# Optimization experiments

Hardware: AMD Instinct MI355X
Metric: run time of the kernel (lower is better)

The kernel has to match this reference:

```python
import jax, jax.numpy as jnp
import numpy as np

NODE_DIM = 256
EDGE_H = 128
B, N = 2, 512
EPS = 1e-5

def _layernorm(x, g, b):
    mu = jnp.mean(x, axis=-1, keepdims=True)
    var = jnp.mean((x - mu) ** 2, axis=-1, keepdims=True)
    return (x - mu) * jax.lax.rsqrt(var + EPS) * g + b

def setup_inputs() -> dict:
    key = jax.random.key(0)
    ks = jax.random.split(key, 12)
    s = lambda k, shape, fan: jax.random.normal(k, shape, jnp.float32) * (1.0 / np.sqrt(fan))
    return {
        "latent_values": jax.random.normal(ks[0], (B, N, NODE_DIM), jnp.float32),
        "sn_g": jnp.ones((NODE_DIM,), jnp.float32),
        "sn_b": jnp.zeros((NODE_DIM,), jnp.float32),
        "tn_g": jnp.ones((NODE_DIM,), jnp.float32),
        "tn_b": jnp.zeros((NODE_DIM,), jnp.float32),
        "sW": s(ks[1], (EDGE_H, NODE_DIM), NODE_DIM),
        "sb": jnp.zeros((EDGE_H,), jnp.float32),
        "tW": s(ks[2], (EDGE_H, NODE_DIM), NODE_DIM),
        "tb": jnp.zeros((EDGE_H,), jnp.float32),
        "W1": s(ks[3], (EDGE_H, 3 * EDGE_H), 3 * EDGE_H),
        "b1": jnp.zeros((EDGE_H,), jnp.float32),
        "W2": s(ks[4], (1, EDGE_H), EDGE_H),
        "b2": jnp.zeros((1,), jnp.float32),
    }

def reference(latent_values, sn_g, sn_b, tn_g, tn_b, sW, sb, tW, tb, W1, b1, W2, b2):
    # projected source/target features: [B, N, H]
    src = _layernorm(latent_values, sn_g, sn_b) @ sW.T + sb
    tgt = _layernorm(latent_values, tn_g, tn_b) @ tW.T + tb
    # first MLP linear on concat([src_i, tgt_j, src_i*tgt_j]) decomposed into
    # three H-blocks of W1 -- same math, no 3H concat materialized.
    Ws, Wt, Wp = W1[:, :EDGE_H], W1[:, EDGE_H:2 * EDGE_H], W1[:, 2 * EDGE_H:]
    h = (src @ Ws.T)[:, :, None, :] + (tgt @ Wt.T)[:, None, :, :]
    h = h + jnp.einsum("bih,bjh,kh->bijk", src, tgt, Wp) + b1  # [B, N, N, H]
    h = jax.nn.gelu(h, approximate=False)
    logits = jnp.einsum("bijk,k->bij", h, W2[0]) + b2[0]
    edges = logits / (1.0 + jnp.abs(logits))  # softsign
    # mask self-edges (allow_self_edges=False)
    diag = jnp.eye(N, dtype=bool)
    return jnp.where(diag[None, :, :], 0.0, edges)
```

## Files before the change

### kernel.cpp

```cpp
#include <hip/hip_runtime.h>
#include <math.h>

#define BN 512
#define ND 256
#define EH 128

typedef __attribute__((ext_vector_type(8))) short short8v;
typedef __attribute__((ext_vector_type(4))) float f32x4;

__device__ __forceinline__ unsigned short f2bf_rn(float x) {
  unsigned int u = __float_as_uint(x);
  unsigned int r = u + 0x7FFFu + ((u >> 16) & 1u);
  return (unsigned short)(r >> 16);
}
__device__ __forceinline__ float bf2f(unsigned short h) {
  return __uint_as_float(((unsigned int)h) << 16);
}

__global__ __launch_bounds__(256) void prep_kernel(
    const float* __restrict__ latent,
    const float* __restrict__ sng, const float* __restrict__ snb,
    const float* __restrict__ tng, const float* __restrict__ tnb,
    const float* __restrict__ sW,  const float* __restrict__ sb,
    const float* __restrict__ tW,  const float* __restrict__ tbv,
    const float* __restrict__ W1,  const float* __restrict__ b1,
    float* __restrict__ srcg, float* __restrict__ apreg,
    unsigned short* __restrict__ tgtb)
{
  __shared__ float lns[4][256];
  __shared__ float lnt[4][256];
  __shared__ float ssrc[4][128];
  const int tid = threadIdx.x;
  const int w = tid >> 6, lane = tid & 63;
  const int row0 = blockIdx.x << 2;

  {
    const int row = row0 + w;
    const float* x = latent + (size_t)row * ND;
    const int h = lane << 2;
    float4 xv = *(const float4*)(x + h);
    float s1 = xv.x + xv.y + xv.z + xv.w;
    float s2 = xv.x*xv.x + xv.y*xv.y + xv.z*xv.z + xv.w*xv.w;
    #pragma unroll
    for (int m = 1; m < 64; m <<= 1) {
      s1 += __shfl_xor(s1, m, 64);
      s2 += __shfl_xor(s2, m, 64);
    }
    const float mu  = s1 * (1.0f/256.0f);
    const float var = s2 * (1.0f/256.0f) - mu*mu;
    const float rstd = rsqrtf(var + 1e-5f);
    float4 ga = *(const float4*)(sng + h), ba = *(const float4*)(snb + h);
    float4 gb = *(const float4*)(tng + h), bb = *(const float4*)(tnb + h);
    const float n0 = (xv.x - mu)*rstd, n1 = (xv.y - mu)*rstd;
    const float n2 = (xv.z - mu)*rstd, n3 = (xv.w - mu)*rstd;
    lns[w][h+0] = n0*ga.x + ba.x; lns[w][h+1] = n1*ga.y + ba.y;
    lns[w][h+2] = n2*ga.z + ba.z; lns[w][h+3] = n3*ga.w + ba.w;
    lnt[w][h+0] = n0*gb.x + bb.x; lnt[w][h+1] = n1*gb.y + bb.y;
    lnt[w][h+2] = n2*gb.z + bb.z; lnt[w][h+3] = n3*gb.w + bb.w;
  }
  __syncthreads();

  const int side = tid >> 7, k = tid & 127;
  {
    const float* W = side ? tW : sW;
    const float bias = side ? tbv[k] : sb[k];
    const float (*L)[256] = side ? lnt : lns;
    float a0 = bias, a1 = bias, a2 = bias, a3 = bias;
    const float* wr = W + (size_t)k * ND;
    for (int h4 = 0; h4 < ND; h4 += 4) {
      float4 wv = *(const float4*)(wr + h4);
      float4 l0 = *(const float4*)&L[0][h4];
      float4 l1 = *(const float4*)&L[1][h4];
      float4 l2 = *(const float4*)&L[2][h4];
      float4 l3 = *(const float4*)&L[3][h4];
      a0 += wv.x*l0.x + wv.y*l0.y + wv.z*l0.z + wv.w*l0.w;
      a1 += wv.x*l1.x + wv.y*l1.y + wv.z*l1.z + wv.w*l1.w;
      a2 += wv.x*l2.x + wv.y*l2.y + wv.z*l2.z + wv.w*l2.w;
      a3 += wv.x*l3.x + wv.y*l3.y + wv.z*l3.z + wv.w*l3.w;
    }
    if (!side) {
      ssrc[0][k]=a0; ssrc[1][k]=a1; ssrc[2][k]=a2; ssrc[3][k]=a3;
      srcg[(size_t)(row0+0)*EH+k]=a0; srcg[(size_t)(row0+1)*EH+k]=a1;
      srcg[(size_t)(row0+2)*EH+k]=a2; srcg[(size_t)(row0+3)*EH+k]=a3;
    } else {
      tgtb[(size_t)(row0+0)*EH + k] = f2bf_rn(a0);
      tgtb[(size_t)(row0+1)*EH + k] = f2bf_rn(a1);
      tgtb[(size_t)(row0+2)*EH + k] = f2bf_rn(a2);
      tgtb[(size_t)(row0+3)*EH + k] = f2bf_rn(a3);
    }
  }
  __syncthreads();

  {
    const int kk = tid & 127, half = tid >> 7;
    const float bb = b1[kk];
    float a0 = bb, a1 = bb;
    const float* wr = W1 + (size_t)kk * 384;
    const int r0 = half * 2;
    for (int h4 = 0; h4 < EH; h4 += 4) {
      float4 wv = *(const float4*)(wr + h4);
      float4 l0 = *(const float4*)&ssrc[r0][h4];
      float4 l1 = *(const float4*)&ssrc[r0+1][h4];
      a0 += wv.x*l0.x + wv.y*l0.y + wv.z*l0.z + wv.w*l0.w;
      a1 += wv.x*l1.x + wv.y*l1.y + wv.z*l1.z + wv.w*l1.w;
    }
    apreg[(size_t)(row0+r0)*EH + kk]   = a0;
    apreg[(size_t)(row0+r0+1)*EH + kk] = a1;
  }
}

__global__ __launch_bounds__(256, 2) void edge_kernel(
    const float* __restrict__ srcg, const float* __restrict__ apreg,
    const unsigned short* __restrict__ tgtb,
    const float* __restrict__ W1, const float* __restrict__ W2,
    const float* __restrict__ b2, float* __restrict__ out)
{
  __shared__ __align__(16) unsigned short Ghi[128 * 128];
  __shared__ __align__(16) unsigned short Glo[128 * 128];
  __shared__ float s_src[128];

  const int tid = threadIdx.x;
  const int l = tid & 63, w = tid >> 6;
  const int blk = blockIdx.x;
  const int b = blk >> 9, i = blk & 511;

  if (tid < 128) s_src[tid] = srcg[(size_t)blk * EH + tid];
  __syncthreads();

  {
    const int k = tid >> 1, h0 = (tid & 1) * 64;
    const float* wpr = W1 + (size_t)k * 384 + 256 + h0;
    const float* wtr = W1 + (size_t)k * 384 + 128 + h0;
    const unsigned int swz = (unsigned int)((k & 15) << 4);
    char* ghB = (char*)Ghi + k * 256;
    char* glB = (char*)Glo + k * 256;
    #pragma unroll
    for (int c = 0; c < 64; c += 8) {
      float4 wpa = *(const float4*)(wpr + c);
      float4 wpb = *(const float4*)(wpr + c + 4);
      float4 wta = *(const float4*)(wtr + c);
      float4 wtb = *(const float4*)(wtr + c + 4);
      float4 sa  = *(const float4*)&s_src[h0 + c];
      float4 sb4 = *(const float4*)&s_src[h0 + c + 4];
      float g[8];
      g[0] = fmaf(sa.x,  wpa.x, wta.x); g[1] = fmaf(sa.y,  wpa.y, wta.y);
      g[2] = fmaf(sa.z,  wpa.z, wta.z); g[3] = fmaf(sa.w,  wpa.w, wta.w);
      g[4] = fmaf(sb4.x, wpb.x, wtb.x); g[5] = fmaf(sb4.y, wpb.y, wtb.y);
      g[6] = fmaf(sb4.z, wpb.z, wtb.z); g[7] = fmaf(sb4.w, wpb.w, wtb.w);
      short8v hv, lv;
      #pragma unroll
      for (int q = 0; q < 8; ++q) {
        unsigned short hh = f2bf_rn(g[q]);
        hv[q] = (short)hh;
        lv[q] = (short)f2bf_rn(g[q] - bf2f(hh));
      }
      const unsigned int off = ((unsigned int)((h0 + c) * 2)) ^ swz;
      *(short8v*)(ghB + off) = hv;
      *(short8v*)(glB + off) = lv;
    }
  }
  __syncthreads();

  const int l15 = l & 15;
  const int hi4 = l >> 4;
  float apv[8], w2h[8];
  #pragma unroll
  for (int nt = 0; nt < 8; ++nt) {
    apv[nt] = apreg[(size_t)blk * EH + nt * 16 + l15];
    w2h[nt] = 0.5f * W2[nt * 16 + l15];
  }
  const float b2s = b2[0];

  const unsigned short* tB = tgtb + (size_t)b * BN * EH;
  float* orow = out + (size_t)blk * BN;

  const int cb = hi4 * 16;
  const unsigned int swzl = (unsigned int)(l15 << 4);

#define LOADA(buf, ks_)                                                        \
  {                                                                            \
    _Pragma("unroll")                                                          \
    for (int m = 0; m < 4; ++m) {                                              \
      const size_t r = (size_t)(jt0 + m * 16 + l15) * EH + (ks_) * 32 + hi4 * 8;\
      buf[m] = *(const short8v*)(tB + r);                                      \
    }                                                                          \
  }

#define MFMA_STEP(buf, ks_)                                                    \
  {                                                                            \
    _Pragma("unroll")                                                          \
    for (int nt = 0; nt < 8; ++nt) {                                           \
      const int rowoff = nt * 4096 + l15 * 256;                                \
      const unsigned int col = ((unsigned int)(((ks_) << 6) | cb)) ^ swzl;     \
      short8v bhi = *(const short8v*)((const char*)Ghi + rowoff + col);        \
      short8v blo = *(const short8v*)((const char*)Glo + rowoff + col);        \
      _Pragma("unroll")                                                        \
      for (int m = 0; m < 4; ++m) {                                            \
        acc[m][nt] = __builtin_amdgcn_mfma_f32_16x16x32_bf16(buf[m], bhi, acc[m][nt], 0, 0, 0); \
        acc[m][nt] = __builtin_amdgcn_mfma_f32_16x16x32_bf16(buf[m], blo, acc[m][nt], 0, 0, 0); \
      }                                                                        \
    }                                                                          \
  }

  #pragma unroll 1
  for (int p = 0; p < 2; ++p) {
    const int jt0 = (w * 8 + p * 4) * 16;
    f32x4 acc[4][8];
    #pragma unroll
    for (int m = 0; m < 4; ++m)
      #pragma unroll
      for (int nt = 0; nt < 8; ++nt)
        acc[m][nt] = (f32x4){0.f, 0.f, 0.f, 0.f};

    short8v aA[4], aB[4];
    LOADA(aA, 0)
    #pragma unroll 1
    for (int kk = 0; kk < 2; ++kk) {
      const int ks0 = kk * 2;
      LOADA(aB, ks0 + 1)
      MFMA_STEP(aA, ks0)
      if (kk == 0) LOADA(aA, 2)
      MFMA_STEP(aB, ks0 + 1)
    }

    #pragma unroll
    for (int m = 0; m < 4; ++m) {
      #pragma unroll
      for (int reg = 0; reg < 4; ++reg) {
        float ps = 0.0f;
        #pragma unroll
        for (int nt = 0; nt < 8; ++nt) {
          const float x = acc[m][nt][reg] + apv[nt];
          const float e  = __builtin_amdgcn_exp2f(x * x * -0.7213475204f);
          const float t  = __builtin_amdgcn_rcpf(fmaf(0.33267817f, fabsf(x), 1.0f));
          const float pl = t * fmaf(t, fmaf(t, 0.7478556f, -0.0958798f), 0.3480242f);
          const float u  = x * (pl * e);
          const float tw = fmaf(2.0f, x, -u);
          const float g2 = (x < 0.0f) ? u : tw;
          ps = fmaf(w2h[nt], g2, ps);
        }
        ps += __shfl_xor(ps, 1, 64);
        ps += __shfl_xor(ps, 2, 64);
        ps += __shfl_xor(ps, 4, 64);
        ps += __shfl_xor(ps, 8, 64);
        if (l15 == 0) {
          const int j = jt0 + m * 16 + hi4 * 4 + reg;
          const float s = ps + b2s;
          const float e2 = s / (1.0f + fabsf(s));
          orow[j] = (j == i) ? 0.0f : e2;
        }
      }
    }
  }
#undef LOADA
#undef MFMA_STEP
}

extern "C" void kernel_launch(void* const* d_in, const int* in_sizes, int n_in,
                              void* d_out, int out_size, void* d_ws, size_t ws_size,
                              hipStream_t stream) {
  const float* latent = (const float*)d_in[0];
  const float* sng = (const float*)d_in[1];
  const float* snb = (const float*)d_in[2];
  const float* tng = (const float*)d_in[3];
  const float* tnb = (const float*)d_in[4];
  const float* sW  = (const float*)d_in[5];
  const float* sb  = (const float*)d_in[6];
  const float* tW  = (const float*)d_in[7];
  const float* tb  = (const float*)d_in[8];
  const float* W1  = (const float*)d_in[9];
  const float* b1  = (const float*)d_in[10];
  const float* W2  = (const float*)d_in[11];
  const float* b2  = (const float*)d_in[12];
  float* out = (float*)d_out;

  float* ws = (float*)d_ws;
  float* srcg  = ws;
  float* apreg = ws + 131072;
  unsigned short* tgtb = (unsigned short*)(ws + 262144);

  hipLaunchKernelGGL(prep_kernel, dim3(256), dim3(256), 0, stream,
                     latent, sng, snb, tng, tnb, sW, sb, tW, tb, W1, b1,
                     srcg, apreg, tgtb);
  hipLaunchKernelGGL(edge_kernel, dim3(1024), dim3(256), 0, stream,
                     srcg, apreg, tgtb, W1, W2, b2, out);
}
```

Before: 84.13 us.

## Drop bf16 hi/lo split, use tanh-approx GELU, shrink tiles for occupancy

Removes the low-order bf16 correction term for the W1-derived B operand, which halves the MFMA count and the LDS footprint. The exact-erf GELU polynomial is replaced by a sigmoid-based tanh approximation. Tiles shrink to 2 M-subtiles with 4 passes, allowing four waves per SIMD, and the apre bias is folded into the accumulator initialisation. Outputs are now written as float4. The cost is lower numerical accuracy from the single bf16 product and the approximate GELU, which may exceed tolerance.

```diff
diff --git a/kernel.cpp b/kernel.cpp
--- a/kernel.cpp
+++ b/kernel.cpp
@@ -109,14 +109,13 @@
   }
 }
 
-__global__ __launch_bounds__(256, 2) void edge_kernel(
+__global__ __launch_bounds__(256, 4) void edge_kernel(
     const float* __restrict__ srcg, const float* __restrict__ apreg,
     const unsigned short* __restrict__ tgtb,
     const float* __restrict__ W1, const float* __restrict__ W2,
     const float* __restrict__ b2, float* __restrict__ out)
 {
-  __shared__ __align__(16) unsigned short Ghi[128 * 128];
-  __shared__ __align__(16) unsigned short Glo[128 * 128];
+  __shared__ __align__(16) unsigned short Gs[128 * 128];
   __shared__ float s_src[128];
 
   const int tid = threadIdx.x;
@@ -132,8 +131,7 @@
     const float* wpr = W1 + (size_t)k * 384 + 256 + h0;
     const float* wtr = W1 + (size_t)k * 384 + 128 + h0;
     const unsigned int swz = (unsigned int)((k & 15) << 4);
-    char* ghB = (char*)Ghi + k * 256;
-    char* glB = (char*)Glo + k * 256;
+    char* gB = (char*)Gs + k * 256;
     #pragma unroll
     for (int c = 0; c < 64; c += 8) {
       float4 wpa = *(const float4*)(wpr + c);
@@ -142,32 +140,28 @@
       float4 wtb = *(const float4*)(wtr + c + 4);
       float4 sa  = *(const float4*)&s_src[h0 + c];
       float4 sb4 = *(const float4*)&s_src[h0 + c + 4];
-      float g[8];
-      g[0] = fmaf(sa.x,  wpa.x, wta.x); g[1] = fmaf(sa.y,  wpa.y, wta.y);
-      g[2] = fmaf(sa.z,  wpa.z, wta.z); g[3] = fmaf(sa.w,  wpa.w, wta.w);
-      g[4] = fmaf(sb4.x, wpb.x, wtb.x); g[5] = fmaf(sb4.y, wpb.y, wtb.y);
-      g[6] = fmaf(sb4.z, wpb.z, wtb.z); g[7] = fmaf(sb4.w, wpb.w, wtb.w);
-      short8v hv, lv;
-      #pragma unroll
-      for (int q = 0; q < 8; ++q) {
-        unsigned short hh = f2bf_rn(g[q]);
-        hv[q] = (short)hh;
-        lv[q] = (short)f2bf_rn(g[q] - bf2f(hh));
-      }
+      short8v hv;
+      hv[0] = (short)f2bf_rn(fmaf(sa.x,  wpa.x, wta.x));
+      hv[1] = (short)f2bf_rn(fmaf(sa.y,  wpa.y, wta.y));
+      hv[2] = (short)f2bf_rn(fmaf(sa.z,  wpa.z, wta.z));
+      hv[3] = (short)f2bf_rn(fmaf(sa.w,  wpa.w, wta.w));
+      hv[4] = (short)f2bf_rn(fmaf(sb4.x, wpb.x, wtb.x));
+      hv[5] = (short)f2bf_rn(fmaf(sb4.y, wpb.y, wtb.y));
+      hv[6] = (short)f2bf_rn(fmaf(sb4.z, wpb.z, wtb.z));
+      hv[7] = (short)f2bf_rn(fmaf(sb4.w, wpb.w, wtb.w));
       const unsigned int off = ((unsigned int)((h0 + c) * 2)) ^ swz;
-      *(short8v*)(ghB + off) = hv;
-      *(short8v*)(glB + off) = lv;
+      *(short8v*)(gB + off) = hv;
     }
   }
   __syncthreads();
 
   const int l15 = l & 15;
   const int hi4 = l >> 4;
-  float apv[8], w2h[8];
+  float apv[8], w2v[8];
   #pragma unroll
   for (int nt = 0; nt < 8; ++nt) {
     apv[nt] = apreg[(size_t)blk * EH + nt * 16 + l15];
-    w2h[nt] = 0.5f * W2[nt * 16 + l15];
+    w2v[nt] = W2[nt * 16 + l15];
   }
   const float b2s = b2[0];
 
@@ -180,7 +174,7 @@
 #define LOADA(buf, ks_)                                                        \
   {                                                                            \
     _Pragma("unroll")                                                          \
-    for (int m = 0; m < 4; ++m) {                                              \
+    for (int m = 0; m < 2; ++m) {                                              \
       const size_t r = (size_t)(jt0 + m * 16 + l15) * EH + (ks_) * 32 + hi4 * 8;\
       buf[m] = *(const short8v*)(tB + r);                                      \
     }                                                                          \
@@ -192,63 +186,62 @@
     for (int nt = 0; nt < 8; ++nt) {                                           \
       const int rowoff = nt * 4096 + l15 * 256;                                \
       const unsigned int col = ((unsigned int)(((ks_) << 6) | cb)) ^ swzl;     \
-      short8v bhi = *(const short8v*)((const char*)Ghi + rowoff + col);        \
-      short8v blo = *(const short8v*)((const char*)Glo + rowoff + col);        \
+      short8v bfr = *(const short8v*)((const char*)Gs + rowoff + col);         \
       _Pragma("unroll")                                                        \
-      for (int m = 0; m < 4; ++m) {                                            \
-        acc[m][nt] = __builtin_amdgcn_mfma_f32_16x16x32_bf16(buf[m], bhi, acc[m][nt], 0, 0, 0); \
-        acc[m][nt] = __builtin_amdgcn_mfma_f32_16x16x32_bf16(buf[m], blo, acc[m][nt], 0, 0, 0); \
-      }                                                                        \
+      for (int m = 0; m < 2; ++m)                                              \
+        acc[m][nt] = __builtin_amdgcn_mfma_f32_16x16x32_bf16(buf[m], bfr, acc[m][nt], 0, 0, 0); \
     }                                                                          \
   }
 
   #pragma unroll 1
-  for (int p = 0; p < 2; ++p) {
-    const int jt0 = (w * 8 + p * 4) * 16;
-    f32x4 acc[4][8];
-    #pragma unroll
-    for (int m = 0; m < 4; ++m)
+  for (int p = 0; p < 4; ++p) {
+    const int jt0 = (p * 8 + w * 2) * 16;
+    f32x4 acc[2][8];
+    #pragma unroll
+    for (int m = 0; m < 2; ++m)
       #pragma unroll
       for (int nt = 0; nt < 8; ++nt)
-        acc[m][nt] = (f32x4){0.f, 0.f, 0.f, 0.f};
-
-    short8v aA[4], aB[4];
+        acc[m][nt] = (f32x4){apv[nt], apv[nt], apv[nt], apv[nt]};
+
+    short8v aA[2], aB[2];
     LOADA(aA, 0)
-    #pragma unroll 1
-    for (int kk = 0; kk < 2; ++kk) {
-      const int ks0 = kk * 2;
-      LOADA(aB, ks0 + 1)
-      MFMA_STEP(aA, ks0)
-      if (kk == 0) LOADA(aA, 2)
-      MFMA_STEP(aB, ks0 + 1)
-    }
-
-    #pragma unroll
-    for (int m = 0; m < 4; ++m) {
+    LOADA(aB, 1)
+    MFMA_STEP(aA, 0)
+    LOADA(aA, 2)
+    MFMA_STEP(aB, 1)
+    LOADA(aB, 3)
+    MFMA_STEP(aA, 2)
+    MFMA_STEP(aB, 3)
+
+    #pragma unroll
+    for (int m = 0; m < 2; ++m) {
+      float ov[4];
       #pragma unroll
       for (int reg = 0; reg < 4; ++reg) {
         float ps = 0.0f;
         #pragma unroll
         for (int nt = 0; nt < 8; ++nt) {
-          const float x = acc[m][nt][reg] + apv[nt];
-          const float e  = __builtin_amdgcn_exp2f(x * x * -0.7213475204f);
-          const float t  = __builtin_amdgcn_rcpf(fmaf(0.33267817f, fabsf(x), 1.0f));
-          const float pl = t * fmaf(t, fmaf(t, 0.7478556f, -0.0958798f), 0.3480242f);
-          const float u  = x * (pl * e);
-          const float tw = fmaf(2.0f, x, -u);
-          const float g2 = (x < 0.0f) ? u : tw;
-          ps = fmaf(w2h[nt], g2, ps);
+          const float x  = acc[m][nt][reg];
+          const float x2 = x * x;
+          const float q   = fmaf(x2, -0.10294817f, -2.3022077f);
+          const float e   = __builtin_amdgcn_exp2f(x * q);
+          const float r   = __builtin_amdgcn_rcpf(1.0f + e);
+          ps = fmaf(w2v[nt], x * r, ps);
         }
         ps += __shfl_xor(ps, 1, 64);
         ps += __shfl_xor(ps, 2, 64);
         ps += __shfl_xor(ps, 4, 64);
         ps += __shfl_xor(ps, 8, 64);
-        if (l15 == 0) {
-          const int j = jt0 + m * 16 + hi4 * 4 + reg;
-          const float s = ps + b2s;
-          const float e2 = s / (1.0f + fabsf(s));
-          orow[j] = (j == i) ? 0.0f : e2;
-        }
+        const float s = ps + b2s;
+        ov[reg] = s / (1.0f + fabsf(s));
+      }
+      if (l15 == 0) {
+        const int j0 = jt0 + m * 16 + hi4 * 4;
+        float4 o4 = {(j0 + 0 == i) ? 0.0f : ov[0],
+                     (j0 + 1 == i) ? 0.0f : ov[1],
+                     (j0 + 2 == i) ? 0.0f : ov[2],
+                     (j0 + 3 == i) ? 0.0f : ov[3]};
+        *(float4*)(orow + j0) = o4;
       }
     }
   }
```

Result: slower. 249.4 us (+196.4%).
